# Kernel optimization log

Measured on AMD Instinct MI355X. Metric: run time of the kernel, lower is better.

The kernel has to match this reference:

```python
import jax, jax.numpy as jnp
import numpy as np

ATOM_VOC = 128
PAD = 0

def setup_inputs() -> dict:
    key = jax.random.key(0)
    ks = jax.random.split(key, 12)
    b, l, d_model, nhead, apo = 8, 256, 512, 16, 128
    atoms = jax.random.randint(ks[0], (b, l), 0, ATOM_VOC)
    chirals = jax.random.randint(ks[1], (b, l), 0, 4)
    coordinates = jax.random.normal(ks[2], (b, l, 3), dtype=jnp.float32)
    bonds = jax.random.randint(ks[3], (b, l, l), 0, 32)
    atype_emb = jax.random.normal(ks[4], (ATOM_VOC, d_model), jnp.float32).at[PAD].set(0.0)
    chiral_emb = jax.random.normal(ks[5], (4, d_model), jnp.float32).at[PAD].set(0.0)
    apair_w_tab = jax.random.normal(ks[6], (ATOM_VOC * ATOM_VOC, apo), jnp.float32)
    apair_b_tab = jax.random.normal(ks[7], (ATOM_VOC * ATOM_VOC, apo), jnp.float32)
    means = jnp.zeros((apo,), jnp.float32)
    stds = jnp.ones((apo,), jnp.float32)
    bond_emb = jax.random.normal(ks[8], (32, nhead), jnp.float32).at[PAD].set(0.0)
    lin_w = jax.random.normal(ks[9], (apo, nhead), jnp.float32) / np.sqrt(apo)
    lin_b = jax.random.normal(ks[10], (nhead,), jnp.float32)
    return dict(atoms=atoms, chirals=chirals, coordinates=coordinates, bonds=bonds,
                atype_emb=atype_emb, chiral_emb=chiral_emb, apair_w_tab=apair_w_tab,
                apair_b_tab=apair_b_tab, means=means, stds=stds, bond_emb=bond_emb,
                lin_w=lin_w, lin_b=lin_b)

def _safe_dist(coordinates):
    # pairwise distances [b,l,l]; safe-sqrt so grad at 0 distance is 0 (diagonal)
    diff = coordinates[:, None, :, :] - coordinates[:, :, None, :]
    s = jnp.sum(diff * diff, axis=-1)
    return jnp.where(s > 0, jnp.sqrt(jnp.where(s > 0, s, 1.0)), 0.0)

def reference(atoms, chirals, coordinates, bonds, atype_emb, chiral_emb,
              apair_w_tab, apair_b_tab, means, stds, bond_emb, lin_w, lin_b):
    # atoms_emb: [l, b, d_model]
    atoms_emb = (atype_emb[atoms] + chiral_emb[chirals]).transpose(1, 0, 2)
    dist = _safe_dist(coordinates)                      # [b,l,l]
    pair_idx = atoms[:, None, :] * ATOM_VOC + atoms[:, :, None]  # [b,l,l]
    ap = apair_w_tab[pair_idx] * dist[..., None] + apair_b_tab[pair_idx]  # [b,l,l,apo]
    std = jnp.abs(stds) + 1e-5
    gauss = jnp.exp(-0.5 * ((ap - means) / std) ** 2) / (np.sqrt(2.0 * np.pi) * std)
    apairs = jnp.einsum('bijk,kh->bijh', gauss, lin_w) + lin_b + bond_emb[bonds]
    pad_mask = (atoms == PAD)[:, None, :, None]         # mask over key/column dim
    apairs = jnp.where(pad_mask, -jnp.inf, apairs)
    return atoms_emb, apairs.transpose(0, 3, 1, 2)      # [b,nhead,l,l]
```

## Files before the change

kernel.cpp:

```cpp
#include <hip/hip_runtime.h>
#include <hip/hip_fp16.h>
#include <math.h>
#include <stdint.h>

#define B 8
#define L 256
#define DM 512
#define NH 16
#define APO 128
#define VOC 128
#define EMB (L * B * DM)

typedef __attribute__((ext_vector_type(8))) _Float16 half8v;
typedef __attribute__((ext_vector_type(4))) float float4v;

#define WSB_BOFF   1024
#define PACK_BOFF  16384
#define PACK_BYTES (128 * 128 * 256)
#define WS_NEED    ((size_t)PACK_BOFF + (size_t)PACK_BYTES)

__device__ __forceinline__ void g2lds16(const void* g, void* l) {
    __builtin_amdgcn_global_load_lds(
        (const __attribute__((address_space(1))) unsigned int*)g,
        (__attribute__((address_space(3))) unsigned int*)l, 16, 0, 0);
}

__global__ __launch_bounds__(256) void pack_kernel(const float* __restrict__ wtab,
                                                   const float* __restrict__ btab,
                                                   const float* __restrict__ means,
                                                   const float* __restrict__ stds,
                                                   const float* __restrict__ lin_w,
                                                   float* __restrict__ ws) {
    const float beta = sqrtf(0.5f * 1.4426950408889634f);
    const float gscale = 0.3989422804014327f;
    int t = threadIdx.x;

    if (blockIdx.x == 0) {
        unsigned short* wsB = (unsigned short*)((char*)ws + WSB_BOFF);
        for (int idx = t; idx < 4 * 64 * 8; idx += 256) {
            int p = idx >> 9;
            int lane = (idx >> 3) & 63;
            int e = idx & 7;
            int k = p * 32 + ((lane >> 4) << 3) + e;
            int h = lane & 15;
            float sigma = fabsf(stds[k]) + 1e-5f;
            float v = lin_w[k * NH + h] * (gscale / sigma);
            __half hv = __float2half(v);
            wsB[idx] = *reinterpret_cast<unsigned short*>(&hv);
        }
    }

    int idx = blockIdx.x * 256 + t;
    int r = idx >> 4;
    int a_i = r >> 7, a_j = r & 127;
    int U = idx & 15;
    int k0 = U * 8;
    size_t src = ((size_t)a_j * VOC + a_i) * APO + k0;
    const float4* w4p = (const float4*)(wtab + src);
    const float4* b4p = (const float4*)(btab + src);
    float4 w0 = w4p[0], w1 = w4p[1], b0 = b4p[0], b1 = b4p[1];
    float wq[8], bq[8];
    #pragma unroll
    for (int e = 0; e < 8; ++e) {
        int k = k0 + e;
        float sigma = fabsf(stds[k]) + 1e-5f;
        float ia = beta / sigma;
        float wvv = ((e < 4) ? ((const float*)&w0)[e] : ((const float*)&w1)[e - 4]) * ia;
        float bvv = (((e < 4) ? ((const float*)&b0)[e] : ((const float*)&b1)[e - 4])
                     - means[k]) * ia;
        wq[e] = wvv; bq[e] = bvv;
    }
    int wlo = 0, whi = 0, blo = 0, bhi = 0;
    wlo = __builtin_amdgcn_cvt_pk_fp8_f32(wq[0], wq[1], wlo, 0);
    wlo = __builtin_amdgcn_cvt_pk_fp8_f32(wq[2], wq[3], wlo, 1);
    whi = __builtin_amdgcn_cvt_pk_fp8_f32(wq[4], wq[5], whi, 0);
    whi = __builtin_amdgcn_cvt_pk_fp8_f32(wq[6], wq[7], whi, 1);
    blo = __builtin_amdgcn_cvt_pk_fp8_f32(bq[0], bq[1], blo, 0);
    blo = __builtin_amdgcn_cvt_pk_fp8_f32(bq[2], bq[3], blo, 1);
    bhi = __builtin_amdgcn_cvt_pk_fp8_f32(bq[4], bq[5], bhi, 0);
    bhi = __builtin_amdgcn_cvt_pk_fp8_f32(bq[6], bq[7], bhi, 1);
    int pu = U ^ (a_j & 15);
    uint4 o;
    o.x = (unsigned)wlo; o.y = (unsigned)whi;
    o.z = (unsigned)blo; o.w = (unsigned)bhi;
    *(uint4*)((char*)ws + PACK_BOFF + (size_t)r * 256 + (size_t)pu * 16) = o;
}

__global__ __launch_bounds__(256, 5) void pair_fused(const int* __restrict__ atoms,
                                                     const int* __restrict__ chirals,
                                                     const float* __restrict__ coords,
                                                     const int* __restrict__ bonds,
                                                     const float* __restrict__ atype,
                                                     const float* __restrict__ chiral,
                                                     const float* __restrict__ bond_emb,
                                                     const float* __restrict__ lin_b,
                                                     const float* __restrict__ ws,
                                                     float* __restrict__ out) {
    __shared__ __align__(16) char stage[32 * 1024];

    int t = threadIdx.x;
    int bid = blockIdx.x;
    int bi = bid >> 8, i = bid & 255;
    int w = t >> 6, l = t & 63;

    int a_i = atoms[bi * L + i];
    int av = atoms[bi * L + t];

    float cix = coords[((size_t)bi * L + i) * 3 + 0];
    float ciy = coords[((size_t)bi * L + i) * 3 + 1];
    float ciz = coords[((size_t)bi * L + i) * 3 + 2];
    float cjx = coords[((size_t)bi * L + t) * 3 + 0];
    float cjy = coords[((size_t)bi * L + t) * 3 + 1];
    float cjz = coords[((size_t)bi * L + t) * 3 + 2];
    float dx = cjx - cix, dy = cjy - ciy, dz = cjz - ciz;
    float s2 = dx * dx + dy * dy + dz * dz;
    float d = (s2 > 0.0f) ? sqrtf(s2) : 0.0f;
    int dbits = __float_as_int(d);

    half8v bfrag[4];
    {
        const uint4* wb = (const uint4*)((const char*)ws + WSB_BOFF);
        #pragma unroll
        for (int p = 0; p < 4; ++p) {
            uint4 r = wb[p * 64 + l];
            bfrag[p] = *reinterpret_cast<half8v*>(&r);
        }
    }

    int m = l >> 4;
    float dval[4];
    int base[4], ax[4];
    #pragma unroll
    for (int q = 0; q < 4; ++q) {
        int idx4 = (q * 16 + (l & 15)) * 4;
        int a = __builtin_amdgcn_ds_bpermute(idx4, av);
        dval[q] = __int_as_float(__builtin_amdgcn_ds_bpermute(idx4, dbits));
        base[q] = a * 256;
        ax[q] = a & 15;
    }

    float4v acc[4];
    #pragma unroll
    for (int q = 0; q < 4; ++q) { float4v z = {0, 0, 0, 0}; acc[q] = z; }

    const char* pkbi = (const char*)ws + PACK_BOFF + (size_t)a_i * 32768;

    asm volatile("s_waitcnt vmcnt(0)" ::: "memory");
    __builtin_amdgcn_sched_barrier(0);
    #pragma unroll
    for (int it = 0; it < 8; ++it) {
        size_t off = (size_t)(w * 32 + it * 4) * 256 + (size_t)l * 16;
        g2lds16(pkbi + off, stage + off);
    }
    asm volatile("s_waitcnt vmcnt(0)" ::: "memory");
    __syncthreads();

    if (t < 128) {
        int a = atoms[bi * L + i];
        int c = chirals[bi * L + i];
        const float4* va = (const float4*)(atype + (size_t)a * DM);
        const float4* vc = (const float4*)(chiral + (size_t)c * DM);
        float4 x = va[t], y = vc[t];
        x.x += y.x; x.y += y.y; x.z += y.z; x.w += y.w;
        ((float4*)(out + ((size_t)i * B + bi) * DM))[t] = x;
    }

    #pragma unroll
    for (int rr = 0; rr < 4; ++rr) {
        #pragma unroll
        for (int q = 0; q < 4; ++q) {
            int un = (rr * 4 + m) ^ ax[q];
            uint4 u = *(const uint4*)(stage + base[q] + (un << 4));
            auto w01 = __builtin_amdgcn_cvt_pk_f32_fp8((int)u.x, 0);
            auto w23 = __builtin_amdgcn_cvt_pk_f32_fp8((int)u.x, 1);
            auto w45 = __builtin_amdgcn_cvt_pk_f32_fp8((int)u.y, 0);
            auto w67 = __builtin_amdgcn_cvt_pk_f32_fp8((int)u.y, 1);
            auto b01 = __builtin_amdgcn_cvt_pk_f32_fp8((int)u.z, 0);
            auto b23 = __builtin_amdgcn_cvt_pk_f32_fp8((int)u.z, 1);
            auto b45 = __builtin_amdgcn_cvt_pk_f32_fp8((int)u.w, 0);
            auto b67 = __builtin_amdgcn_cvt_pk_f32_fp8((int)u.w, 1);
            float dq = dval[q];
            float t0 = fmaf(w01[0], dq, b01[0]);
            float t1 = fmaf(w01[1], dq, b01[1]);
            float t2 = fmaf(w23[0], dq, b23[0]);
            float t3 = fmaf(w23[1], dq, b23[1]);
            float t4 = fmaf(w45[0], dq, b45[0]);
            float t5 = fmaf(w45[1], dq, b45[1]);
            float t6 = fmaf(w67[0], dq, b67[0]);
            float t7 = fmaf(w67[1], dq, b67[1]);
            float g0 = __builtin_amdgcn_exp2f(-(t0 * t0));
            float g1 = __builtin_amdgcn_exp2f(-(t1 * t1));
            float g2 = __builtin_amdgcn_exp2f(-(t2 * t2));
            float g3 = __builtin_amdgcn_exp2f(-(t3 * t3));
            float g4 = __builtin_amdgcn_exp2f(-(t4 * t4));
            float g5 = __builtin_amdgcn_exp2f(-(t5 * t5));
            float g6 = __builtin_amdgcn_exp2f(-(t6 * t6));
            float g7 = __builtin_amdgcn_exp2f(-(t7 * t7));
            auto p0 = __builtin_amdgcn_cvt_pkrtz(g0, g1);
            auto p1 = __builtin_amdgcn_cvt_pkrtz(g2, g3);
            auto p2 = __builtin_amdgcn_cvt_pkrtz(g4, g5);
            auto p3 = __builtin_amdgcn_cvt_pkrtz(g6, g7);
            uint4 au;
            au.x = *reinterpret_cast<unsigned*>(&p0);
            au.y = *reinterpret_cast<unsigned*>(&p1);
            au.z = *reinterpret_cast<unsigned*>(&p2);
            au.w = *reinterpret_cast<unsigned*>(&p3);
            half8v af = *reinterpret_cast<half8v*>(&au);
            acc[q] = __builtin_amdgcn_mfma_f32_16x16x32_f16(af, bfrag[rr],
                                                            acc[q], 0, 0, 0);
        }
    }

    asm volatile("s_waitcnt lgkmcnt(0)" ::: "memory");
    __syncthreads();

    int a_j = atoms[bi * L + t];
    int bvd = bonds[(((size_t)bi * L) + i) * L + t];
    float beh[NH];
    {
        const float4* ber = (const float4*)(bond_emb + (size_t)bvd * NH);
        #pragma unroll
        for (int u = 0; u < 4; ++u) {
            float4 v4 = ber[u];
            beh[u * 4 + 0] = v4.x; beh[u * 4 + 1] = v4.y;
            beh[u * 4 + 2] = v4.z; beh[u * 4 + 3] = v4.w;
        }
    }
    float* cbuf = (float*)(stage + (size_t)w * 4352);
    {
        int h = l & 15, jg = l >> 4;
        #pragma unroll
        for (int q = 0; q < 4; ++q)
            *(float4v*)(cbuf + h * 68 + q * 16 + jg * 4) = acc[q];
    }
    asm volatile("s_waitcnt lgkmcnt(0)" ::: "memory");
    __builtin_amdgcn_sched_barrier(0);

    size_t obase = (((size_t)bi * NH) * L + i) * L + t;
    float ninf = __uint_as_float(0xff7f0000u);
    bool pad = (a_j == 0);
    #pragma unroll
    for (int h = 0; h < NH; ++h) {
        float v = cbuf[h * 68 + l] + lin_b[h] + beh[h];
        out[(size_t)EMB + obase + (size_t)h * L * L] = pad ? ninf : v;
    }
}

extern "C" void kernel_launch(void* const* d_in, const int* in_sizes, int n_in,
                              void* d_out, int out_size, void* d_ws, size_t ws_size,
                              hipStream_t stream) {
    const int*   atoms    = (const int*)d_in[0];
    const int*   chirals  = (const int*)d_in[1];
    const float* coords   = (const float*)d_in[2];
    const int*   bonds    = (const int*)d_in[3];
    const float* atype    = (const float*)d_in[4];
    const float* chiral   = (const float*)d_in[5];
    const float* wtab     = (const float*)d_in[6];
    const float* btab     = (const float*)d_in[7];
    const float* means    = (const float*)d_in[8];
    const float* stds     = (const float*)d_in[9];
    const float* bond_emb = (const float*)d_in[10];
    const float* lin_w    = (const float*)d_in[11];
    const float* lin_b    = (const float*)d_in[12];
    float* out = (float*)d_out;
    float* ws  = (float*)d_ws;

    pack_kernel<<<1024, 256, 0, stream>>>(wtab, btab, means, stds, lin_w, ws);
    pair_fused<<<B * L, 256, 0, stream>>>(atoms, chirals, coords, bonds,
                                          atype, chiral, bond_emb, lin_b, ws, out);
}
```

Baseline: 33.02 us.

## Schedule pair blocks by atom type to improve L2 reuse of packed tables

Block 0 of the pack kernel now counting-sorts all (batch,row) indices by atom type and writes the resulting order into the workspace. The fused pair kernel then maps block ids through that order, interleaved across 8 slots, so blocks that read the same 32KB packed slice for a given atom type are in flight together and can share it in cache. It also removes a full vmcnt wait and sched barrier ahead of the LDS staging loads. The cost is extra serial work in block 0 of the pack kernel, one more dependent load at the start of each pair block, and an output write order that is no longer sequential.

```diff
diff --git a/kernel.cpp b/kernel.cpp
--- a/kernel.cpp
+++ b/kernel.cpp
@@ -15,7 +15,8 @@
 typedef __attribute__((ext_vector_type(4))) float float4v;
 
 #define WSB_BOFF   1024
-#define PACK_BOFF  16384
+#define ORD_BOFF   9216
+#define PACK_BOFF  24576
 #define PACK_BYTES (128 * 128 * 256)
 #define WS_NEED    ((size_t)PACK_BOFF + (size_t)PACK_BYTES)
 
@@ -30,6 +31,7 @@
                                                    const float* __restrict__ means,
                                                    const float* __restrict__ stds,
                                                    const float* __restrict__ lin_w,
+                                                   const int* __restrict__ atoms,
                                                    float* __restrict__ ws) {
     const float beta = sqrtf(0.5f * 1.4426950408889634f);
     const float gscale = 0.3989422804014327f;
@@ -47,6 +49,24 @@
             float v = lin_w[k * NH + h] * (gscale / sigma);
             __half hv = __float2half(v);
             wsB[idx] = *reinterpret_cast<unsigned short*>(&hv);
+        }
+        __shared__ int hist[128];
+        if (t < 128) hist[t] = 0;
+        __syncthreads();
+        for (int vb = t; vb < 2048; vb += 256)
+            atomicAdd(&hist[atoms[vb] & 127], 1);
+        __syncthreads();
+        __shared__ int offs[128];
+        if (t == 0) {
+            int acc = 0;
+            for (int bkt = 0; bkt < 128; ++bkt) { offs[bkt] = acc; acc += hist[bkt]; }
+        }
+        __syncthreads();
+        int* order = (int*)((char*)ws + ORD_BOFF);
+        for (int vb = t; vb < 2048; vb += 256) {
+            int a = atoms[vb] & 127;
+            int pos = atomicAdd(&offs[a], 1);
+            order[pos] = vb;
         }
     }
 
@@ -99,8 +119,10 @@
     __shared__ __align__(16) char stage[32 * 1024];
 
     int t = threadIdx.x;
-    int bid = blockIdx.x;
-    int bi = bid >> 8, i = bid & 255;
+    int p = blockIdx.x;
+    const int* order = (const int*)((const char*)ws + ORD_BOFF);
+    int vb = order[(p & 7) * 256 + (p >> 3)];
+    int bi = vb >> 8, i = vb & 255;
     int w = t >> 6, l = t & 63;
 
     int a_i = atoms[bi * L + i];
@@ -121,9 +143,9 @@
     {
         const uint4* wb = (const uint4*)((const char*)ws + WSB_BOFF);
         #pragma unroll
-        for (int p = 0; p < 4; ++p) {
-            uint4 r = wb[p * 64 + l];
-            bfrag[p] = *reinterpret_cast<half8v*>(&r);
+        for (int pp = 0; pp < 4; ++pp) {
+            uint4 r = wb[pp * 64 + l];
+            bfrag[pp] = *reinterpret_cast<half8v*>(&r);
         }
     }
 
@@ -145,8 +167,6 @@
 
     const char* pkbi = (const char*)ws + PACK_BOFF + (size_t)a_i * 32768;
 
-    asm volatile("s_waitcnt vmcnt(0)" ::: "memory");
-    __builtin_amdgcn_sched_barrier(0);
     #pragma unroll
     for (int it = 0; it < 8; ++it) {
         size_t off = (size_t)(w * 32 + it * 4) * 256 + (size_t)l * 16;
@@ -265,7 +285,7 @@
     float* out = (float*)d_out;
     float* ws  = (float*)d_ws;
 
-    pack_kernel<<<1024, 256, 0, stream>>>(wtab, btab, means, stds, lin_w, ws);
+    pack_kernel<<<1024, 256, 0, stream>>>(wtab, btab, means, stds, lin_w, atoms, ws);
     pair_fused<<<B * L, 256, 0, stream>>>(atoms, chirals, coords, bonds,
                                           atype, chiral, bond_emb, lin_b, ws, out);
 }
```

After: 32.62 us (median of 2 runs). No clear change (-1.2%).
